# Performance work log

Measured on AMD Instinct MI355X. Metric: run time of the kernel, lower is better.

Reference implementation:

```python
import jax, jax.numpy as jnp
import numpy as np

B, N, D, H = 32, 4096, 768, 384

def setup_inputs() -> dict:
    key = jax.random.key(0)
    k1, k2, k3 = jax.random.split(key, 3)
    patch_tokens = jax.random.normal(k1, (B, N, D), dtype=jnp.float32)
    # score head params (kaiming-like scale)
    w1 = jax.random.normal(k2, (D, H), dtype=jnp.float32) * (2.0 / H) ** 0.5
    b1 = jnp.zeros((H,), dtype=jnp.float32)
    w2 = jax.random.normal(k3, (H,), dtype=jnp.float32) * (2.0 / 1) ** 0.5
    b2 = jnp.zeros((), dtype=jnp.float32)
    return {"patch_tokens": patch_tokens, "w1": w1, "b1": b1, "w2": w2, "b2": b2,
            "keep_ratio_pct": 50}

def reference(patch_tokens, w1, b1, w2, b2, keep_ratio_pct):
    # score head: Linear -> GELU (erf variant, torch default) -> Linear(->1)
    h = jax.nn.gelu(jnp.einsum('bnd,dh->bnh', patch_tokens, w1) + b1, approximate=False)
    patch_logits = jnp.einsum('bnh,h->bn', h, w2) + b2                 # [B, N]
    foreground_scores = jax.nn.sigmoid(patch_logits)                    # [B, N]

    patch_count = patch_tokens.shape[1]
    keep_count = max(1, int(patch_count * keep_ratio_pct / 100))
    keep_count = min(keep_count, patch_count)

    if keep_count == patch_count:
        keep_mask = jnp.ones_like(foreground_scores)
    else:
        topk_scores, _ = jax.lax.top_k(foreground_scores, keep_count)   # [B, k], sorted desc
        keep_threshold = jax.lax.stop_gradient(topk_scores[:, -1:])     # [B, 1]
        keep_mask = (foreground_scores >= keep_threshold).astype(foreground_scores.dtype)

    filtered_scores = foreground_scores * keep_mask
    filtered_weights = filtered_scores / (jnp.sum(filtered_scores, axis=1, keepdims=True) + 1e-12)
    filtered_feat = jnp.einsum('bn,bnd->bd', filtered_weights, patch_tokens)  # [B, D]
    return (filtered_feat, filtered_weights, foreground_scores, keep_mask)
```

## Files before the change

kernel.cpp:

```cpp
#include <hip/hip_runtime.h>
#include <math.h>

#define BB 32
#define NN 4096
#define DD 768
#define HH 384
#define NCH 8

typedef _Float16 half8 __attribute__((ext_vector_type(8)));
typedef __fp16 fp16x2 __attribute__((ext_vector_type(2)));
typedef float f32x4 __attribute__((ext_vector_type(4)));

__global__ __launch_bounds__(64) void fapf_prep_w(
    const float* __restrict__ w1, short* __restrict__ whf, short* __restrict__ wlf)
{
    const int cf = blockIdx.x;
    const int kg = blockIdx.y;
    const int l  = threadIdx.x;
    const int c  = cf * 16 + (l & 15);
    const int kb = kg * 32 + (l >> 4) * 8;

    short hs[8], ls[8];
#pragma unroll
    for (int i = 0; i < 8; i++) {
        float v = w1[(size_t)(kb + i) * HH + c];
        _Float16 hi = (_Float16)v;
        _Float16 lo = (_Float16)(v - (float)hi);
        hs[i] = *(short*)&hi;
        ls[i] = *(short*)&lo;
    }
    size_t base = ((size_t)(kg * 24 + cf) * 64 + l) * 8;
#pragma unroll
    for (int i = 0; i < 8; i++) { whf[base + i] = hs[i]; wlf[base + i] = ls[i]; }
}

__global__ __launch_bounds__(256)
__attribute__((amdgpu_waves_per_eu(2)))
void fapf_scores_mfma(
    const float* __restrict__ x, const short* __restrict__ whf,
    const short* __restrict__ wlf, const float* __restrict__ b1,
    const float* __restrict__ w2, const float* __restrict__ b2,
    float* __restrict__ scores)
{
    __shared__ __align__(16) short xh[2][32 * 64];
    __shared__ __align__(16) short xl[2][32 * 64];
    __shared__ float part[32][4];

    const int tid = threadIdx.x;
    const int l   = tid & 63;
    const int cw  = tid >> 6;
    const int t0  = blockIdx.x * 32;

    f32x4 acc[2][6];
#pragma unroll
    for (int fr = 0; fr < 2; fr++)
#pragma unroll
        for (int cf = 0; cf < 6; cf++) acc[fr][cf] = (f32x4){0.f, 0.f, 0.f, 0.f};

    const half8* whp = (const half8*)whf + (size_t)(cw * 6) * 64 + l;
    const half8* wlp = (const half8*)wlf + (size_t)(cw * 6) * 64 + l;

    float4 xv[2];

#define LOADX(ch)                                                            \
    {                                                                        \
        _Pragma("unroll")                                                    \
        for (int it = 0; it < 2; it++) {                                     \
            int id = it * 256 + tid;                                         \
            xv[it] = *(const float4*)&x[(size_t)(t0 + (id >> 4)) * DD        \
                                        + (ch) * 64 + (id & 15) * 4];        \
        }                                                                    \
    }

#define SPLITWRITE(buf)                                                      \
    {                                                                        \
        _Pragma("unroll")                                                    \
        for (int it = 0; it < 2; it++) {                                     \
            int id = it * 256 + tid;                                         \
            int row = id >> 4, seg = id & 15;                                \
            float vv[4] = {xv[it].x, xv[it].y, xv[it].z, xv[it].w};          \
            union { fp16x2 h; unsigned int u; float f; } h0, h1, p0, p1;     \
            h0.h = __builtin_amdgcn_cvt_pkrtz(vv[0], vv[1]);                 \
            h1.h = __builtin_amdgcn_cvt_pkrtz(vv[2], vv[3]);                 \
            float l0 = vv[0] - (float)h0.h[0];                               \
            float l1 = vv[1] - (float)h0.h[1];                               \
            float l2 = vv[2] - (float)h1.h[0];                               \
            float l3 = vv[3] - (float)h1.h[1];                               \
            p0.h = __builtin_amdgcn_cvt_pkrtz(l0, l1);                       \
            p1.h = __builtin_amdgcn_cvt_pkrtz(l2, l3);                       \
            uint2 uh, ul;                                                    \
            uh.x = h0.u; uh.y = h1.u;                                        \
            ul.x = p0.u; ul.y = p1.u;                                        \
            int idx = (row * 64 + seg * 4) ^ ((row & 7) << 3);               \
            *(uint2*)&xh[buf][idx] = uh;                                     \
            *(uint2*)&xl[buf][idx] = ul;                                     \
        }                                                                    \
    }

#define LOADB(dst, ptr, kg)                                                  \
    {                                                                        \
        _Pragma("unroll")                                                    \
        for (int cf = 0; cf < 6; cf++)                                       \
            dst[cf] = (ptr)[(size_t)(kg) * 1536 + (size_t)cf * 64];          \
    }

    half8 b[3][6];
    half8 ah[2], al[2];

    LOADX(0);
    SPLITWRITE(0);
    LOADB(b[0], whp, 0);
    LOADB(b[1], wlp, 0);
    __syncthreads();
    LOADX(1);

    for (int sc = 0; sc < 4; sc++) {
#pragma unroll
        for (int cc = 0; cc < 3; cc++) {
            const int c   = sc * 3 + cc;
            const int cur = c & 1;
#pragma unroll
            for (int tp = 0; tp < 4; tp++) {
                const int tloc  = cc * 4 + tp;
                const int u     = tloc % 3;
                const int ui    = (tloc + 2) % 3;
                const int kind  = tp & 1;
                const int ks    = tp >> 1;
                const int kindi = (tloc + 2) & 1;

                int kgi = (sc * 12 + tloc + 2) >> 1;
                if (kgi > 23) kgi = 23;
                if (kindi == 0) { LOADB(b[ui], whp, kgi); }
                else            { LOADB(b[ui], wlp, kgi); }

                if (kind == 0) {
#pragma unroll
                    for (int fr = 0; fr < 2; fr++) {
                        int row = fr * 16 + (l & 15);
                        int idx = (row * 64 + ks * 32 + (l >> 4) * 8)
                                  ^ ((row & 7) << 3);
                        ah[fr] = *(const half8*)&xh[cur][idx];
                        al[fr] = *(const half8*)&xl[cur][idx];
                    }
                    __builtin_amdgcn_s_setprio(1);
#pragma unroll
                    for (int fr = 0; fr < 2; fr++)
#pragma unroll
                        for (int cf = 0; cf < 6; cf++)
                            acc[fr][cf] = __builtin_amdgcn_mfma_f32_16x16x32_f16(
                                ah[fr], b[u][cf], acc[fr][cf], 0, 0, 0);
#pragma unroll
                    for (int fr = 0; fr < 2; fr++)
#pragma unroll
                        for (int cf = 0; cf < 6; cf++)
                            acc[fr][cf] = __builtin_amdgcn_mfma_f32_16x16x32_f16(
                                al[fr], b[u][cf], acc[fr][cf], 0, 0, 0);
                    __builtin_amdgcn_s_setprio(0);
                } else {
                    __builtin_amdgcn_s_setprio(1);
#pragma unroll
                    for (int fr = 0; fr < 2; fr++)
#pragma unroll
                        for (int cf = 0; cf < 6; cf++)
                            acc[fr][cf] = __builtin_amdgcn_mfma_f32_16x16x32_f16(
                                ah[fr], b[u][cf], acc[fr][cf], 0, 0, 0);
                    __builtin_amdgcn_s_setprio(0);
                }
            }

            if (c < 11) {
                SPLITWRITE(cur ^ 1);
                __syncthreads();
                if (c < 10) LOADX(c + 2);
            }
        }
    }

    float b1v[6], w2v[6];
#pragma unroll
    for (int cf = 0; cf < 6; cf++) {
        int col = cw * 96 + cf * 16 + (l & 15);
        b1v[cf] = b1[col];
        w2v[cf] = w2[col];
    }
    float p[2][4];
#pragma unroll
    for (int fr = 0; fr < 2; fr++)
#pragma unroll
        for (int j = 0; j < 4; j++) p[fr][j] = 0.f;
#pragma unroll
    for (int fr = 0; fr < 2; fr++)
#pragma unroll
        for (int cf = 0; cf < 6; cf++)
#pragma unroll
            for (int j = 0; j < 4; j++) {
                float hh = acc[fr][cf][j] + b1v[cf];
                float g  = 0.5f * hh * (1.f + erff(hh * 0.70710678118654752f));
                p[fr][j] = fmaf(g, w2v[cf], p[fr][j]);
            }
#pragma unroll
    for (int m = 8; m >= 1; m >>= 1)
#pragma unroll
        for (int fr = 0; fr < 2; fr++)
#pragma unroll
            for (int j = 0; j < 4; j++)
                p[fr][j] += __shfl_xor(p[fr][j], m, 64);

    if ((l & 15) == 0) {
#pragma unroll
        for (int fr = 0; fr < 2; fr++)
#pragma unroll
            for (int j = 0; j < 4; j++) {
                int row = fr * 16 + (l >> 4) * 4 + j;
                part[row][cw] = p[fr][j];
            }
    }
    __syncthreads();
    if (tid < 32) {
        float lg = part[tid][0] + part[tid][1] + part[tid][2] + part[tid][3] + b2[0];
        scores[t0 + tid] = 1.f / (1.f + expf(-lg));
    }
#undef LOADX
#undef SPLITWRITE
#undef LOADB
}

__global__ __launch_bounds__(1024) void fapf_select_kernel(
    const float* __restrict__ scores, const int* __restrict__ pct_p,
    float* __restrict__ weights, float* __restrict__ mask,
    float* __restrict__ feat, int* __restrict__ kidx,
    float* __restrict__ kw, int* __restrict__ kcnt)
{
    __shared__ float s[NN];
    __shared__ float red[1024];
    __shared__ int scnt;
    const int b = blockIdx.x, tid = threadIdx.x;

    if (tid == 0) scnt = 0;
    for (int i = tid; i < DD; i += 1024) feat[b * DD + i] = 0.f;
    for (int i = tid; i < NN; i += 1024) s[i] = scores[b * NN + i];
    __syncthreads();

    for (int k = 2; k <= NN; k <<= 1) {
        for (int j = k >> 1; j > 0; j >>= 1) {
            for (int i = tid; i < NN; i += 1024) {
                int ixj = i ^ j;
                if (ixj > i) {
                    bool up = ((i & k) == 0);
                    float a = s[i], c = s[ixj];
                    if (up ? (a > c) : (a < c)) { s[i] = c; s[ixj] = a; }
                }
            }
            __syncthreads();
        }
    }

    int pct = pct_p[0];
    long long kcl = (long long)NN * pct / 100;
    int kc = (int)kcl;
    if (kc < 1) kc = 1;
    if (kc > NN) kc = NN;
    float thr = s[NN - kc];

    float local = 0.f;
    for (int i = tid; i < NN; i += 1024) {
        float v = scores[b * NN + i];
        if (v >= thr) local += v;
    }
    red[tid] = local;
    __syncthreads();
    for (int step = 512; step > 0; step >>= 1) {
        if (tid < step) red[tid] += red[tid + step];
        __syncthreads();
    }
    float inv = 1.f / (red[0] + 1e-12f);
    const int lane = tid & 63;
    for (int i = tid; i < NN; i += 1024) {
        float v = scores[b * NN + i];
        bool keep = (v >= thr);
        float m = keep ? 1.f : 0.f;
        weights[b * NN + i] = v * m * inv;
        mask[b * NN + i]    = m;
        if (kidx) {
            unsigned long long bal = __ballot(keep);
            int base = 0;
            if (lane == 0) base = atomicAdd(&scnt, __popcll(bal));
            base = __shfl(base, 0, 64);
            if (keep) {
                int off = __popcll(bal & ((1ULL << lane) - 1ULL));
                kidx[b * NN + base + off] = i;
                kw[b * NN + base + off]   = v * inv;
            }
        }
    }
    if (kidx) {
        __syncthreads();
        if (tid == 0) kcnt[b] = scnt;
    }
}

__global__ __launch_bounds__(256) void fapf_feat_compact(
    const float* __restrict__ x, const int* __restrict__ kidx,
    const float* __restrict__ kw, const int* __restrict__ kcnt,
    float* __restrict__ feat)
{
    const int b  = blockIdx.y;
    const int d0 = blockIdx.x * 64;
    const int ch = blockIdx.z;
    const int dl = threadIdx.x & 63;
    const int ng = threadIdx.x >> 6;

    const int cnt = kcnt[b];
    int per = (cnt + NCH - 1) / NCH;
    int j0 = ch * per; if (j0 > cnt) j0 = cnt;
    int j1 = j0 + per; if (j1 > cnt) j1 = cnt;
    int len = j1 - j0;
    int per_w = (len + 3) >> 2;
    int s = j0 + ng * per_w;
    int e = s + per_w; if (e > j1) e = j1;

    const float* xb  = x + (size_t)b * NN * DD + d0 + dl;
    const int*   ib  = kidx + b * NN;
    const float* wbp = kw + b * NN;

    float a[8];
#pragma unroll
    for (int u = 0; u < 8; u++) a[u] = 0.f;

    int j = s;
    for (; j + 8 <= e; j += 8) {
        int   idx[8];
        float ww[8];
#pragma unroll
        for (int u = 0; u < 8; u++) { idx[u] = ib[j + u]; ww[u] = wbp[j + u]; }
#pragma unroll
        for (int u = 0; u < 8; u++)
            a[u] = fmaf(ww[u], xb[(size_t)idx[u] * DD], a[u]);
    }
    for (; j < e; j++)
        a[0] = fmaf(wbp[j], xb[(size_t)ib[j] * DD], a[0]);

    float acc = ((a[0] + a[1]) + (a[2] + a[3])) + ((a[4] + a[5]) + (a[6] + a[7]));

    __shared__ float red[4][64];
    red[ng][dl] = acc;
    __syncthreads();
    if (threadIdx.x < 64) {
        float v = (red[0][dl] + red[1][dl]) + (red[2][dl] + red[3][dl]);
        atomicAdd(&feat[b * DD + d0 + dl], v);
    }
}

__global__ __launch_bounds__(256) void fapf_feat_dense(
    const float* __restrict__ x, const float* __restrict__ weights,
    float* __restrict__ feat)
{
    const int b  = blockIdx.y;
    const int d0 = blockIdx.x * 64;
    const int dl = threadIdx.x & 63;
    const int ng = threadIdx.x >> 6;

    const float* xb = x + (size_t)b * NN * DD;
    const float* wb = weights + b * NN;

    float a0 = 0.f, a1 = 0.f, a2 = 0.f, a3 = 0.f;
    for (int n = ng; n < NN; n += 16) {
        float w0 = wb[n], w1v = wb[n + 4], w2v = wb[n + 8], w3 = wb[n + 12];
        float v0 = xb[(size_t)(n)      * DD + d0 + dl];
        float v1 = xb[(size_t)(n + 4)  * DD + d0 + dl];
        float v2 = xb[(size_t)(n + 8)  * DD + d0 + dl];
        float v3 = xb[(size_t)(n + 12) * DD + d0 + dl];
        a0 = fmaf(w0, v0, a0);
        a1 = fmaf(w1v, v1, a1);
        a2 = fmaf(w2v, v2, a2);
        a3 = fmaf(w3, v3, a3);
    }
    float acc = (a0 + a1) + (a2 + a3);

    __shared__ float red[4][64];
    red[ng][dl] = acc;
    __syncthreads();
    if (threadIdx.x < 64) {
        feat[b * DD + d0 + dl] =
            (red[0][dl] + red[1][dl]) + (red[2][dl] + red[3][dl]);
    }
}

extern "C" void kernel_launch(void* const* d_in, const int* in_sizes, int n_in,
                              void* d_out, int out_size, void* d_ws, size_t ws_size,
                              hipStream_t stream) {
    const float* x   = (const float*)d_in[0];
    const float* w1  = (const float*)d_in[1];
    const float* b1  = (const float*)d_in[2];
    const float* w2  = (const float*)d_in[3];
    const float* b2  = (const float*)d_in[4];
    const int*   pct = (const int*)d_in[5];

    float* out = (float*)d_out;
    float* feat    = out;
    float* weights = out + BB * DD;
    float* scores  = weights + BB * NN;
    float* mask    = scores + BB * NN;

    short* whf  = (short*)d_ws;
    short* wlf  = whf + 24 * 24 * 64 * 8;
    int*   kidx = (int*)(wlf + 24 * 24 * 64 * 8);
    float* kw   = (float*)(kidx + BB * NN);
    int*   kcnt = (int*)(kw + BB * NN);

    const size_t needed = 2 * (size_t)(24 * 24 * 64 * 8) * sizeof(short)
                        + (size_t)BB * NN * (sizeof(int) + sizeof(float))
                        + BB * sizeof(int);
    const bool compact = ws_size >= needed;

    fapf_prep_w<<<dim3(24, 24), dim3(64), 0, stream>>>(w1, whf, wlf);
    fapf_scores_mfma<<<dim3(BB * NN / 32), dim3(256), 0, stream>>>(
        x, whf, wlf, b1, w2, b2, scores);
    fapf_select_kernel<<<dim3(BB), dim3(1024), 0, stream>>>(
        scores, pct, weights, mask, feat,
        compact ? kidx : (int*)nullptr, kw, kcnt);
    if (compact) {
        fapf_feat_compact<<<dim3(DD / 64, BB, NCH), dim3(256), 0, stream>>>(
            x, kidx, kw, kcnt, feat);
    } else {
        fapf_feat_dense<<<dim3(DD / 64, BB), dim3(256), 0, stream>>>(
            x, weights, feat);
    }
}
```

Measured before the change: 360.8 us.

## Split hidden dim across two blocks with 64-token tiles and partial logits

The score kernel now gives each block 64 tokens and half of the hidden columns (grid y=2) instead of 32 tokens and all 384 columns. Each block writes partial logits to workspace, and the select kernel adds the two halves, applies b2 and the sigmoid, and keeps the scores in shared memory instead of re-reading them from global. This cuts per-token weight-fragment traffic and register pressure per wave. In exchange, every x row is now loaded and split by two blocks, and the workspace grows by two logit planes.

```diff
diff --git a/kernel.cpp b/kernel.cpp
--- a/kernel.cpp
+++ b/kernel.cpp
@@ -39,33 +39,34 @@
 void fapf_scores_mfma(
     const float* __restrict__ x, const short* __restrict__ whf,
     const short* __restrict__ wlf, const float* __restrict__ b1,
-    const float* __restrict__ w2, const float* __restrict__ b2,
-    float* __restrict__ scores)
+    const float* __restrict__ w2,
+    float* __restrict__ logit_part)
 {
-    __shared__ __align__(16) short xh[2][32 * 64];
-    __shared__ __align__(16) short xl[2][32 * 64];
-    __shared__ float part[32][4];
+    __shared__ __align__(16) short xh[2][64 * 64];
+    __shared__ __align__(16) short xl[2][64 * 64];
+    __shared__ float part[64][4];
 
     const int tid = threadIdx.x;
     const int l   = tid & 63;
     const int cw  = tid >> 6;
-    const int t0  = blockIdx.x * 32;
-
-    f32x4 acc[2][6];
-#pragma unroll
-    for (int fr = 0; fr < 2; fr++)
-#pragma unroll
-        for (int cf = 0; cf < 6; cf++) acc[fr][cf] = (f32x4){0.f, 0.f, 0.f, 0.f};
-
-    const half8* whp = (const half8*)whf + (size_t)(cw * 6) * 64 + l;
-    const half8* wlp = (const half8*)wlf + (size_t)(cw * 6) * 64 + l;
-
-    float4 xv[2];
+    const int t0  = blockIdx.x * 64;
+    const int hf  = blockIdx.y;
+
+    f32x4 acc[4][3];
+#pragma unroll
+    for (int fr = 0; fr < 4; fr++)
+#pragma unroll
+        for (int cf = 0; cf < 3; cf++) acc[fr][cf] = (f32x4){0.f, 0.f, 0.f, 0.f};
+
+    const half8* whp = (const half8*)whf + (size_t)(hf * 12 + cw * 3) * 64 + l;
+    const half8* wlp = (const half8*)wlf + (size_t)(hf * 12 + cw * 3) * 64 + l;
+
+    float4 xv[4];
 
 #define LOADX(ch)                                                            \
     {                                                                        \
         _Pragma("unroll")                                                    \
-        for (int it = 0; it < 2; it++) {                                     \
+        for (int it = 0; it < 4; it++) {                                     \
             int id = it * 256 + tid;                                         \
             xv[it] = *(const float4*)&x[(size_t)(t0 + (id >> 4)) * DD        \
                                         + (ch) * 64 + (id & 15) * 4];        \
@@ -75,11 +76,11 @@
 #define SPLITWRITE(buf)                                                      \
     {                                                                        \
         _Pragma("unroll")                                                    \
-        for (int it = 0; it < 2; it++) {                                     \
+        for (int it = 0; it < 4; it++) {                                     \
             int id = it * 256 + tid;                                         \
             int row = id >> 4, seg = id & 15;                                \
             float vv[4] = {xv[it].x, xv[it].y, xv[it].z, xv[it].w};          \
-            union { fp16x2 h; unsigned int u; float f; } h0, h1, p0, p1;     \
+            union { fp16x2 h; unsigned int u; } h0, h1, p0, p1;              \
             h0.h = __builtin_amdgcn_cvt_pkrtz(vv[0], vv[1]);                 \
             h1.h = __builtin_amdgcn_cvt_pkrtz(vv[2], vv[3]);                 \
             float l0 = vv[0] - (float)h0.h[0];                               \
@@ -100,12 +101,12 @@
 #define LOADB(dst, ptr, kg)                                                  \
     {                                                                        \
         _Pragma("unroll")                                                    \
-        for (int cf = 0; cf < 6; cf++)                                       \
+        for (int cf = 0; cf < 3; cf++)                                       \
             dst[cf] = (ptr)[(size_t)(kg) * 1536 + (size_t)cf * 64];          \
     }
 
-    half8 b[3][6];
-    half8 ah[2], al[2];
+    half8 b[3][3];
+    half8 ah[4], al[4];
 
     LOADX(0);
     SPLITWRITE(0);
@@ -135,7 +136,7 @@
 
                 if (kind == 0) {
 #pragma unroll
-                    for (int fr = 0; fr < 2; fr++) {
+                    for (int fr = 0; fr < 4; fr++) {
                         int row = fr * 16 + (l & 15);
                         int idx = (row * 64 + ks * 32 + (l >> 4) * 8)
                                   ^ ((row & 7) << 3);
@@ -144,24 +145,24 @@
                     }
                     __builtin_amdgcn_s_setprio(1);
 #pragma unroll
-                    for (int fr = 0; fr < 2; fr++)
-#pragma unroll
-                        for (int cf = 0; cf < 6; cf++)
+                    for (int fr = 0; fr < 4; fr++)
+#pragma unroll
+                        for (int cf = 0; cf < 3; cf++)
                             acc[fr][cf] = __builtin_amdgcn_mfma_f32_16x16x32_f16(
                                 ah[fr], b[u][cf], acc[fr][cf], 0, 0, 0);
 #pragma unroll
-                    for (int fr = 0; fr < 2; fr++)
-#pragma unroll
-                        for (int cf = 0; cf < 6; cf++)
+                    for (int fr = 0; fr < 4; fr++)
+#pragma unroll
+                        for (int cf = 0; cf < 3; cf++)
                             acc[fr][cf] = __builtin_amdgcn_mfma_f32_16x16x32_f16(
                                 al[fr], b[u][cf], acc[fr][cf], 0, 0, 0);
                     __builtin_amdgcn_s_setprio(0);
                 } else {
                     __builtin_amdgcn_s_setprio(1);
 #pragma unroll
-                    for (int fr = 0; fr < 2; fr++)
-#pragma unroll
-                        for (int cf = 0; cf < 6; cf++)
+                    for (int fr = 0; fr < 4; fr++)
+#pragma unroll
+                        for (int cf = 0; cf < 3; cf++)
                             acc[fr][cf] = __builtin_amdgcn_mfma_f32_16x16x32_f16(
                                 ah[fr], b[u][cf], acc[fr][cf], 0, 0, 0);
                     __builtin_amdgcn_s_setprio(0);
@@ -176,22 +177,22 @@
         }
     }
 
-    float b1v[6], w2v[6];
-#pragma unroll
-    for (int cf = 0; cf < 6; cf++) {
-        int col = cw * 96 + cf * 16 + (l & 15);
+    float b1v[3], w2v[3];
+#pragma unroll
+    for (int cf = 0; cf < 3; cf++) {
+        int col = hf * 192 + cw * 48 + cf * 16 + (l & 15);
         b1v[cf] = b1[col];
         w2v[cf] = w2[col];
     }
-    float p[2][4];
-#pragma unroll
-    for (int fr = 0; fr < 2; fr++)
+    float p[4][4];
+#pragma unroll
+    for (int fr = 0; fr < 4; fr++)
 #pragma unroll
         for (int j = 0; j < 4; j++) p[fr][j] = 0.f;
 #pragma unroll
-    for (int fr = 0; fr < 2; fr++)
-#pragma unroll
-        for (int cf = 0; cf < 6; cf++)
+    for (int fr = 0; fr < 4; fr++)
+#pragma unroll
+        for (int cf = 0; cf < 3; cf++)
 #pragma unroll
             for (int j = 0; j < 4; j++) {
                 float hh = acc[fr][cf][j] + b1v[cf];
@@ -201,14 +202,14 @@
 #pragma unroll
     for (int m = 8; m >= 1; m >>= 1)
 #pragma unroll
-        for (int fr = 0; fr < 2; fr++)
+        for (int fr = 0; fr < 4; fr++)
 #pragma unroll
             for (int j = 0; j < 4; j++)
                 p[fr][j] += __shfl_xor(p[fr][j], m, 64);
 
     if ((l & 15) == 0) {
 #pragma unroll
-        for (int fr = 0; fr < 2; fr++)
+        for (int fr = 0; fr < 4; fr++)
 #pragma unroll
             for (int j = 0; j < 4; j++) {
                 int row = fr * 16 + (l >> 4) * 4 + j;
@@ -216,9 +217,9 @@
             }
     }
     __syncthreads();
-    if (tid < 32) {
-        float lg = part[tid][0] + part[tid][1] + part[tid][2] + part[tid][3] + b2[0];
-        scores[t0 + tid] = 1.f / (1.f + expf(-lg));
+    if (tid < 64) {
+        logit_part[(size_t)hf * BB * NN + t0 + tid] =
+            part[tid][0] + part[tid][1] + part[tid][2] + part[tid][3];
     }
 #undef LOADX
 #undef SPLITWRITE
@@ -226,19 +227,28 @@
 }
 
 __global__ __launch_bounds__(1024) void fapf_select_kernel(
-    const float* __restrict__ scores, const int* __restrict__ pct_p,
-    float* __restrict__ weights, float* __restrict__ mask,
-    float* __restrict__ feat, int* __restrict__ kidx,
-    float* __restrict__ kw, int* __restrict__ kcnt)
+    const float* __restrict__ logit_part, const float* __restrict__ b2,
+    const int* __restrict__ pct_p,
+    float* __restrict__ scores, float* __restrict__ weights,
+    float* __restrict__ mask, float* __restrict__ feat,
+    int* __restrict__ kidx, float* __restrict__ kw, int* __restrict__ kcnt)
 {
     __shared__ float s[NN];
+    __shared__ float o[NN];
     __shared__ float red[1024];
     __shared__ int scnt;
     const int b = blockIdx.x, tid = threadIdx.x;
+    const float b2v = b2[0];
 
     if (tid == 0) scnt = 0;
     for (int i = tid; i < DD; i += 1024) feat[b * DD + i] = 0.f;
-    for (int i = tid; i < NN; i += 1024) s[i] = scores[b * NN + i];
+    for (int i = tid; i < NN; i += 1024) {
+        float lg = logit_part[b * NN + i] + logit_part[(size_t)BB * NN + b * NN + i] + b2v;
+        float sig = 1.f / (1.f + expf(-lg));
+        s[i] = sig;
+        o[i] = sig;
+        scores[b * NN + i] = sig;
+    }
     __syncthreads();
 
     for (int k = 2; k <= NN; k <<= 1) {
@@ -264,7 +274,7 @@
 
     float local = 0.f;
     for (int i = tid; i < NN; i += 1024) {
-        float v = scores[b * NN + i];
+        float v = o[i];
         if (v >= thr) local += v;
     }
     red[tid] = local;
@@ -276,7 +286,7 @@
     float inv = 1.f / (red[0] + 1e-12f);
     const int lane = tid & 63;
     for (int i = tid; i < NN; i += 1024) {
-        float v = scores[b * NN + i];
+        float v = o[i];
         bool keep = (v >= thr);
         float m = keep ? 1.f : 0.f;
         weights[b * NN + i] = v * m * inv;
@@ -402,22 +412,24 @@
     float* scores  = weights + BB * NN;
     float* mask    = scores + BB * NN;
 
-    short* whf  = (short*)d_ws;
-    short* wlf  = whf + 24 * 24 * 64 * 8;
-    int*   kidx = (int*)(wlf + 24 * 24 * 64 * 8);
-    float* kw   = (float*)(kidx + BB * NN);
-    int*   kcnt = (int*)(kw + BB * NN);
+    short* whf   = (short*)d_ws;
+    short* wlf   = whf + 24 * 24 * 64 * 8;
+    float* logit = (float*)(wlf + 24 * 24 * 64 * 8);
+    int*   kidx  = (int*)(logit + 2 * BB * NN);
+    float* kw    = (float*)(kidx + BB * NN);
+    int*   kcnt  = (int*)(kw + BB * NN);
 
     const size_t needed = 2 * (size_t)(24 * 24 * 64 * 8) * sizeof(short)
+                        + (size_t)2 * BB * NN * sizeof(float)
                         + (size_t)BB * NN * (sizeof(int) + sizeof(float))
                         + BB * sizeof(int);
     const bool compact = ws_size >= needed;
 
     fapf_prep_w<<<dim3(24, 24), dim3(64), 0, stream>>>(w1, whf, wlf);
-    fapf_scores_mfma<<<dim3(BB * NN / 32), dim3(256), 0, stream>>>(
-        x, whf, wlf, b1, w2, b2, scores);
+    fapf_scores_mfma<<<dim3(BB * NN / 64, 2), dim3(256), 0, stream>>>(
+        x, whf, wlf, b1, w2, logit);
     fapf_select_kernel<<<dim3(BB), dim3(1024), 0, stream>>>(
-        scores, pct, weights, mask, feat,
+        logit, b2, pct, scores, weights, mask, feat,
         compact ? kidx : (int*)nullptr, kw, kcnt);
     if (compact) {
         fapf_feat_compact<<<dim3(DD / 64, BB, NCH), dim3(256), 0, stream>>>(
```

Measured after the change: 367.5 us. No clear change (+1.8%).
